# Performance work log

Measured on AMD Instinct MI355X. Metric: run time of the kernel, lower is better.

## Reference

```python
import jax, jax.numpy as jnp
import numpy as np

BN_EPS = 1e-5

def _bn(y, g, b, m, v):
    # inference-mode BatchNorm2d over channel axis 1
    scale = g / jnp.sqrt(v + BN_EPS)
    return (y - m[None, :, None, None]) * scale[None, :, None, None] + b[None, :, None, None]

def setup_inputs() -> dict:
    key = jax.random.key(0)
    ks = jax.random.split(key, 16)
    b, c, h, w = 4, 64, 256, 512
    kc = 32
    return {
        "x": jax.random.normal(ks[0], (b, c, h, w), dtype=jnp.float32),
        "Wq": jax.random.normal(ks[1], (kc, c), dtype=jnp.float32) * 0.05,
        "bnq_g": jax.random.uniform(ks[2], (kc,), dtype=jnp.float32),
        "bnq_b": jax.random.normal(ks[3], (kc,), dtype=jnp.float32) * 0.1,
        "bnq_m": jax.random.normal(ks[4], (kc,), dtype=jnp.float32) * 0.1,
        "bnq_v": jax.random.uniform(ks[5], (kc,), dtype=jnp.float32) + 0.5,
        "Wk": jax.random.normal(ks[6], (kc, c), dtype=jnp.float32) * 0.05,
        "bnk_g": jax.random.uniform(ks[7], (kc,), dtype=jnp.float32),
        "bnk_b": jax.random.normal(ks[8], (kc,), dtype=jnp.float32) * 0.1,
        "bnk_m": jax.random.normal(ks[9], (kc,), dtype=jnp.float32) * 0.1,
        "bnk_v": jax.random.uniform(ks[10], (kc,), dtype=jnp.float32) + 0.5,
        "Wv": jax.random.normal(ks[11], (c, c), dtype=jnp.float32) * 0.05,
        "bv": jax.random.normal(ks[12], (c,), dtype=jnp.float32) * 0.1,
        "gamma": jax.random.normal(ks[13], (1,), dtype=jnp.float32) * 0.1,
    }

def reference(x, Wq, bnq_g, bnq_b, bnq_m, bnq_v, Wk, bnk_g, bnk_b, bnk_m, bnk_v, Wv, bv, gamma):
    # x: [b,c,h,w]. Vertical (height-axis) attention, independent per (batch, column).
    q = _bn(jnp.einsum('kc,bchw->bkhw', Wq, x), bnq_g, bnq_b, bnq_m, bnq_v)  # [b,kc,h,w]
    k = _bn(jnp.einsum('kc,bchw->bkhw', Wk, x), bnk_g, bnk_b, bnk_m, bnk_v)  # [b,kc,h,w]
    # score1 = Q[b,w,h,kc] @ K[b,w,kc,h] -> [b,w,h,h]
    score = jnp.einsum('bkhw,bkgw->bwhg', q, k)
    attn = jax.nn.softmax(score, axis=-1)  # softmax over key height g
    v = jnp.einsum('dc,bchw->bdhw', Wv, x) + bv[None, :, None, None]  # [b,c,h,w]
    buf = jnp.einsum('bwhg,bdgw->bdhw', attn, v)  # [b,c,h,w]
    return gamma * buf + x  # out_add branch
```

## Files before the change

### kernel.cpp

```cpp
#include <hip/hip_runtime.h>
#include <hip/hip_bf16.h>

#define BB 4
#define CC 64
#define HH 256
#define WW 512
#define KCC 32
#define PLANE (HH*WW)

typedef __attribute__((ext_vector_type(8))) __bf16 bf16x8;
typedef __attribute__((ext_vector_type(4))) __bf16 bf16x4;
typedef __attribute__((ext_vector_type(2))) __bf16 bf16x2;
typedef __attribute__((ext_vector_type(4))) float floatx4;

__device__ __forceinline__ float bf2f(unsigned short u) {
    union { unsigned v; float f; } x; x.v = ((unsigned)u) << 16; return x.f;
}

__global__ __launch_bounds__(256, 4)
void proj_kernel(const float* __restrict__ x,
                 const float* __restrict__ Wq, const float* __restrict__ Wk,
                 const float* __restrict__ Wv, const float* __restrict__ bv,
                 const float* __restrict__ bnq_g, const float* __restrict__ bnq_b,
                 const float* __restrict__ bnq_m, const float* __restrict__ bnq_v,
                 const float* __restrict__ bnk_g, const float* __restrict__ bnk_b,
                 const float* __restrict__ bnk_m, const float* __restrict__ bnk_v,
                 unsigned short* __restrict__ Qb, unsigned short* __restrict__ Kb,
                 unsigned short* __restrict__ Vb)
{
    __shared__ __align__(16) unsigned short sX[8 * 256 * 8];
    __shared__ __align__(16) unsigned short sY[4][16 * 40];
    __shared__ float sScale[128], sBias[128];

    const int tid  = threadIdx.x;
    const int lane = tid & 63, wv = tid >> 6;
    const int quad = lane >> 4, lr = lane & 15;
    const int bid  = blockIdx.x;
    const int b = bid >> 9, chunk = bid & 511;
    const int h = chunk >> 1, w0 = (chunk & 1) << 8;

    if (tid < 128) {
        float s, bia;
        if (tid < 32)      { s = bnq_g[tid] * rsqrtf(bnq_v[tid] + 1e-5f); bia = bnq_b[tid] - bnq_m[tid] * s; }
        else if (tid < 64) { int i = tid - 32; s = bnk_g[i] * rsqrtf(bnk_v[i] + 1e-5f); bia = bnk_b[i] - bnk_m[i] * s; }
        else               { s = 1.f; bia = bv[tid - 64]; }
        sScale[tid] = s; sBias[tid] = bia;
    }

    {
        const float* xb = x + (size_t)b * CC * PLANE + h * WW + w0 + tid;
#pragma unroll
        for (int cc = 0; cc < 8; ++cc) {
            bf16x8 v;
#pragma unroll
            for (int j = 0; j < 8; ++j) v[j] = (__bf16)xb[(size_t)(cc * 8 + j) * PLANE];
            *(bf16x8*)&sX[(cc * 256 + tid) * 8] = v;
        }
    }
    __syncthreads();

    const float* Wsrc = (wv == 0) ? Wq : (wv == 1) ? Wk : (Wv + (wv - 2) * 32 * CC);
    bf16x8 wf[2][2];
#pragma unroll
    for (int mt = 0; mt < 2; ++mt)
#pragma unroll
        for (int ks = 0; ks < 2; ++ks) {
            const float* p = Wsrc + (mt * 16 + lr) * CC + ks * 32 + quad * 8;
            bf16x8 v;
#pragma unroll
            for (int j = 0; j < 8; ++j) v[j] = (__bf16)p[j];
            wf[mt][ks] = v;
        }
    float s8[2][4], b8[2][4];
#pragma unroll
    for (int mt = 0; mt < 2; ++mt)
#pragma unroll
        for (int i = 0; i < 4; ++i) {
            int chn = wv * 32 + mt * 16 + quad * 4 + i;
            s8[mt][i] = sScale[chn]; b8[mt][i] = sBias[chn];
        }

    unsigned short* sYw = sY[wv];
    const int p2 = lane >> 2, seg = lane & 3;

    for (int nt = 0; nt < 16; ++nt) {
        bf16x8 xb0 = *(const bf16x8*)&sX[((0 + quad) * 256 + nt * 16 + lr) * 8];
        bf16x8 xb1 = *(const bf16x8*)&sX[((4 + quad) * 256 + nt * 16 + lr) * 8];
#pragma unroll
        for (int mt = 0; mt < 2; ++mt) {
            floatx4 acc = {0.f, 0.f, 0.f, 0.f};
            acc = __builtin_amdgcn_mfma_f32_16x16x32_bf16(wf[mt][0], xb0, acc, 0, 0, 0);
            acc = __builtin_amdgcn_mfma_f32_16x16x32_bf16(wf[mt][1], xb1, acc, 0, 0, 0);
            bf16x4 y;
#pragma unroll
            for (int i = 0; i < 4; ++i) y[i] = (__bf16)(acc[i] * s8[mt][i] + b8[mt][i]);
            *(bf16x4*)&sYw[lr * 40 + mt * 16 + quad * 4] = y;
        }
        uint4 v = *(const uint4*)&sYw[p2 * 40 + seg * 8];
        int w_ = w0 + nt * 16 + p2;
        if (wv == 0)      *(uint4*)&Qb[(size_t)((b * WW + w_) * HH + h) * KCC + seg * 8] = v;
        else if (wv == 1) *(uint4*)&Kb[(size_t)((b * WW + w_) * HH + h) * KCC + seg * 8] = v;
        else              *(uint4*)&Vb[(size_t)((b * WW + w_) * HH + h) * CC + (wv - 2) * 32 + seg * 8] = v;
    }
}

__global__ __launch_bounds__(512, 4)
void attn_kernel(const unsigned short* __restrict__ Qb,
                 const unsigned short* __restrict__ Kb,
                 const unsigned short* __restrict__ Vb,
                 const float* __restrict__ gamma,
                 unsigned short* __restrict__ Ob)
{
    __shared__ __align__(16) unsigned short sVf[16384];
    __shared__ __align__(16) unsigned short sP[8][1280];
    __shared__ float sL[256];

    const int tid = threadIdx.x, lane = tid & 63, wv = tid >> 6;
    const int quad = lane >> 4, lr = lane & 15;
    const int col = blockIdx.x;

    const unsigned short* Qg = Qb + (size_t)col * HH * KCC;
    const unsigned short* Kg = Kb + (size_t)col * HH * KCC;
    const unsigned short* Vg = Vb + (size_t)col * HH * CC;

    bf16x8 qf[2], kf[16];
#pragma unroll
    for (int ht = 0; ht < 2; ++ht)
        qf[ht] = *(const bf16x8*)&Qg[(wv * 32 + ht * 16 + lr) * KCC + quad * 8];
#pragma unroll
    for (int gt = 0; gt < 16; ++gt)
        kf[gt] = *(const bf16x8*)&Kg[(gt * 16 + lr) * KCC + quad * 8];

    unsigned short* sVp = &sP[0][0];
    for (int half = 0; half < 2; ++half) {
#pragma unroll
        for (int it = 0; it < 2; ++it) {
            int idx = it * 512 + tid;
            int gr = idx >> 3, sg = idx & 7;
            *(uint4*)&sVp[gr * CC + sg * 8] =
                *(const uint4*)&Vg[(size_t)(half * 128 + gr) * CC + sg * 8];
        }
        __syncthreads();
#pragma unroll
        for (int it = 0; it < 2; ++it) {
            int id = it * 512 + tid;
            int go = id >> 6, d = id & 63;
            bf16x8 v;
#pragma unroll
            for (int j = 0; j < 8; ++j)
                ((unsigned short*)&v)[j] = sVp[(go * 8 + j) * CC + d];
            *(bf16x8*)&sVf[((half * 16 + go) * 64 + d) * 8] = v;
        }
        __syncthreads();
    }

    floatx4 O[2][4];
#pragma unroll
    for (int a = 0; a < 2; ++a)
#pragma unroll
        for (int dd = 0; dd < 4; ++dd) O[a][dd] = (floatx4){0.f, 0.f, 0.f, 0.f};
    float lpart[2] = {0.f, 0.f};

    unsigned short* sPw = sP[wv];
    const floatx4 zed = {0.f, 0.f, 0.f, 0.f};

#pragma unroll
    for (int ch = 0; ch < 8; ++ch) {
#pragma unroll
        for (int gt = 0; gt < 2; ++gt) {
#pragma unroll
            for (int ht = 0; ht < 2; ++ht) {
                floatx4 s = __builtin_amdgcn_mfma_f32_16x16x32_bf16(kf[ch * 2 + gt], qf[ht], zed, 0, 0, 0);
                float p0 = __expf(s[0]), p1 = __expf(s[1]), p2 = __expf(s[2]), p3 = __expf(s[3]);
                lpart[ht] += (p0 + p1) + (p2 + p3);
                bf16x2 pa = {(__bf16)p0, (__bf16)p1};
                bf16x2 pb = {(__bf16)p2, (__bf16)p3};
                int base = (ht * 16 + lr) * 40 + gt * 16 + quad * 4;
                *(bf16x2*)&sPw[base]     = pa;
                *(bf16x2*)&sPw[base + 2] = pb;
            }
        }
        bf16x8 paf[2];
#pragma unroll
        for (int ht = 0; ht < 2; ++ht)
            paf[ht] = *(const bf16x8*)&sPw[(ht * 16 + lr) * 40 + quad * 8];
#pragma unroll
        for (int dt = 0; dt < 4; ++dt) {
            bf16x8 vf = *(const bf16x8*)&sVf[((ch * 4 + quad) * 64 + dt * 16 + lr) * 8];
#pragma unroll
            for (int ht = 0; ht < 2; ++ht)
                O[ht][dt] = __builtin_amdgcn_mfma_f32_16x16x32_bf16(paf[ht], vf, O[ht][dt], 0, 0, 0);
        }
    }

    const float gm = gamma[0];
#pragma unroll
    for (int ht = 0; ht < 2; ++ht) {
        float l = lpart[ht];
        l += __shfl_xor(l, 16, 64);
        l += __shfl_xor(l, 32, 64);
        if (lane < 16) sL[wv * 32 + ht * 16 + lane] = gm / l;
    }

#pragma unroll
    for (int ht = 0; ht < 2; ++ht) {
        float f0 = sL[wv * 32 + ht * 16 + quad * 4 + 0];
        float f1 = sL[wv * 32 + ht * 16 + quad * 4 + 1];
        float f2 = sL[wv * 32 + ht * 16 + quad * 4 + 2];
        float f3 = sL[wv * 32 + ht * 16 + quad * 4 + 3];
#pragma unroll
        for (int dt = 0; dt < 4; ++dt) {
            floatx4 o = O[ht][dt];
            int cb = dt * 16 + lr;
            *(__bf16*)&sPw[(quad * 4 + 0) * 72 + cb] = (__bf16)(o[0] * f0);
            *(__bf16*)&sPw[(quad * 4 + 1) * 72 + cb] = (__bf16)(o[1] * f1);
            *(__bf16*)&sPw[(quad * 4 + 2) * 72 + cb] = (__bf16)(o[2] * f2);
            *(__bf16*)&sPw[(quad * 4 + 3) * 72 + cb] = (__bf16)(o[3] * f3);
        }
#pragma unroll
        for (int it = 0; it < 2; ++it) {
            int idx = it * 64 + lane;
            int hr = idx >> 3, sg = idx & 7;
            uint4 v = *(const uint4*)&sPw[hr * 72 + sg * 8];
            *(uint4*)&Ob[(size_t)(col * HH + wv * 32 + ht * 16 + hr) * CC + sg * 8] = v;
        }
    }
}

__global__ __launch_bounds__(256)
void add_kernel(const unsigned short* __restrict__ Ob,
                const float* __restrict__ x,
                float* __restrict__ out)
{
    __shared__ __align__(16) unsigned short sT[64 * 72];
    const int tid = threadIdx.x;
    const int bid = blockIdx.x;
    const int b = bid >> 11, rem = bid & 2047, h = rem >> 3, w0 = (rem & 7) << 6;

#pragma unroll
    for (int it = 0; it < 2; ++it) {
        int idx = it * 256 + tid;
        int tw = idx >> 3, sg = idx & 7;
        uint4 v = *(const uint4*)&Ob[(size_t)((b * WW + w0 + tw) * HH + h) * CC + sg * 8];
        *(uint4*)&sT[tw * 72 + sg * 8] = v;
    }
    __syncthreads();

    const int d = tid >> 2, ws = tid & 3;
    const size_t base = ((size_t)(b * CC + d)) * PLANE + h * WW + w0 + ws * 16;
    const float* xp = x + base;
    float* op = out + base;
#pragma unroll
    for (int k = 0; k < 4; ++k) {
        float4 xv = *(const float4*)&xp[k * 4];
        float4 r;
        r.x = bf2f(sT[(ws * 16 + k * 4 + 0) * 72 + d]) + xv.x;
        r.y = bf2f(sT[(ws * 16 + k * 4 + 1) * 72 + d]) + xv.y;
        r.z = bf2f(sT[(ws * 16 + k * 4 + 2) * 72 + d]) + xv.z;
        r.w = bf2f(sT[(ws * 16 + k * 4 + 3) * 72 + d]) + xv.w;
        *(float4*)&op[k * 4] = r;
    }
}

#define KSTR 40
#define VSTR 72
__device__ __forceinline__ float bflo(unsigned u) { union { unsigned v; float f; } x; x.v = u << 16; return x.f; }
__device__ __forceinline__ float bfhi(unsigned u) { union { unsigned v; float f; } x; x.v = u & 0xffff0000u; return x.f; }

__global__ __launch_bounds__(256, 1)
void vattn_fused(const float* __restrict__ x,
                 const float* __restrict__ Wq,
                 const float* __restrict__ bnq_g, const float* __restrict__ bnq_b,
                 const float* __restrict__ bnq_m, const float* __restrict__ bnq_v,
                 const float* __restrict__ Wk,
                 const float* __restrict__ bnk_g, const float* __restrict__ bnk_b,
                 const float* __restrict__ bnk_m, const float* __restrict__ bnk_v,
                 const float* __restrict__ Wv, const float* __restrict__ bv,
                 const float* __restrict__ gamma,
                 float* __restrict__ out)
{
    __shared__ __align__(16) __hip_bfloat16 sK[HH * KSTR];
    __shared__ __align__(16) __hip_bfloat16 sV2[HH * VSTR];
    const int t = threadIdx.x;
    const int bw = blockIdx.x;
    const int b = bw / WW, w = bw % WW;
    const size_t plane = (size_t)HH * WW;
    const float* xp = x + (size_t)b * CC * plane + (size_t)t * WW + w;
    float xr[CC];
#pragma unroll
    for (int c = 0; c < CC; ++c) xr[c] = xp[(size_t)c * plane];
    float qr[KCC];
#pragma unroll
    for (int j = 0; j < KCC; ++j) {
        float aq = 0.f, ak = 0.f;
#pragma unroll
        for (int c = 0; c < CC; ++c) { aq += Wq[j * CC + c] * xr[c]; ak += Wk[j * CC + c] * xr[c]; }
        const float sq = bnq_g[j] * rsqrtf(bnq_v[j] + 1e-5f);
        const float sk = bnk_g[j] * rsqrtf(bnk_v[j] + 1e-5f);
        qr[j] = (aq - bnq_m[j]) * sq + bnq_b[j];
        sK[t * KSTR + j] = __float2bfloat16((ak - bnk_m[j]) * sk + bnk_b[j]);
    }
#pragma unroll
    for (int d = 0; d < CC; ++d) {
        float av = bv[d];
#pragma unroll
        for (int c = 0; c < CC; ++c) av += Wv[d * CC + c] * xr[c];
        sV2[t * VSTR + d] = __float2bfloat16(av);
    }
    __syncthreads();
    float o[CC];
#pragma unroll
    for (int d = 0; d < CC; ++d) o[d] = 0.f;
    float l = 0.f;
    for (int g = 0; g < HH; ++g) {
        const uint4* kp = (const uint4*)(sK + g * KSTR);
        float s = 0.f;
#pragma unroll
        for (int i = 0; i < 4; ++i) {
            const uint4 kk = kp[i];
            s += bflo(kk.x) * qr[i * 8 + 0] + bfhi(kk.x) * qr[i * 8 + 1]
               + bflo(kk.y) * qr[i * 8 + 2] + bfhi(kk.y) * qr[i * 8 + 3]
               + bflo(kk.z) * qr[i * 8 + 4] + bfhi(kk.z) * qr[i * 8 + 5]
               + bflo(kk.w) * qr[i * 8 + 6] + bfhi(kk.w) * qr[i * 8 + 7];
        }
        const float p = __expf(s);
        l += p;
        const uint4* vp = (const uint4*)(sV2 + g * VSTR);
#pragma unroll
        for (int i = 0; i < 8; ++i) {
            const uint4 vv = vp[i];
            o[i * 8 + 0] += p * bflo(vv.x); o[i * 8 + 1] += p * bfhi(vv.x);
            o[i * 8 + 2] += p * bflo(vv.y); o[i * 8 + 3] += p * bfhi(vv.y);
            o[i * 8 + 4] += p * bflo(vv.z); o[i * 8 + 5] += p * bfhi(vv.z);
            o[i * 8 + 6] += p * bflo(vv.w); o[i * 8 + 7] += p * bfhi(vv.w);
        }
    }
    const float gm = gamma[0];
    const float rl = 1.f / l;
    float* op = out + (size_t)b * CC * plane + (size_t)t * WW + w;
#pragma unroll
    for (int d = 0; d < CC; ++d) op[(size_t)d * plane] = gm * (o[d] * rl) + xr[d];
}

extern "C" void kernel_launch(void* const* d_in, const int* in_sizes, int n_in,
                              void* d_out, int out_size, void* d_ws, size_t ws_size,
                              hipStream_t stream) {
    const float* x     = (const float*)d_in[0];
    const float* Wq    = (const float*)d_in[1];
    const float* bnq_g = (const float*)d_in[2];
    const float* bnq_b = (const float*)d_in[3];
    const float* bnq_m = (const float*)d_in[4];
    const float* bnq_v = (const float*)d_in[5];
    const float* Wk    = (const float*)d_in[6];
    const float* bnk_g = (const float*)d_in[7];
    const float* bnk_b = (const float*)d_in[8];
    const float* bnk_m = (const float*)d_in[9];
    const float* bnk_v = (const float*)d_in[10];
    const float* Wv    = (const float*)d_in[11];
    const float* bv    = (const float*)d_in[12];
    const float* gamma = (const float*)d_in[13];
    float* out = (float*)d_out;

    const size_t need = 201326592;
    if (ws_size >= need) {
        unsigned short* Qb = (unsigned short*)d_ws;
        unsigned short* Kb = Qb + 16777216;
        unsigned short* Vb = Kb + 16777216;
        unsigned short* Ob = Vb + 33554432;
        hipLaunchKernelGGL(proj_kernel, dim3(2048), dim3(256), 0, stream,
                           x, Wq, Wk, Wv, bv,
                           bnq_g, bnq_b, bnq_m, bnq_v,
                           bnk_g, bnk_b, bnk_m, bnk_v,
                           Qb, Kb, Vb);
        hipLaunchKernelGGL(attn_kernel, dim3(2048), dim3(512), 0, stream,
                           Qb, Kb, Vb, gamma, Ob);
        hipLaunchKernelGGL(add_kernel, dim3(8192), dim3(256), 0, stream,
                           Ob, x, out);
    } else {
        hipLaunchKernelGGL(vattn_fused, dim3(BB * WW), dim3(HH), 0, stream,
                           x, Wq, bnq_g, bnq_b, bnq_m, bnq_v,
                           Wk, bnk_g, bnk_b, bnk_m, bnk_v,
                           Wv, bv, gamma, out);
    }
}
```

Measured before the change: 423.5 us.

## Tile projection kernel over 16x16 spatial blocks for contiguous Q/K/V stores

```diff
diff --git a/kernel.cpp b/kernel.cpp
--- a/kernel.cpp
+++ b/kernel.cpp
@@ -29,40 +29,37 @@
                  unsigned short* __restrict__ Vb)
 {
     __shared__ __align__(16) unsigned short sX[8 * 256 * 8];
-    __shared__ __align__(16) unsigned short sY[4][16 * 40];
-    __shared__ float sScale[128], sBias[128];
+    __shared__ __align__(16) unsigned short sYQ[16 * 40];
+    __shared__ __align__(16) unsigned short sYK[16 * 40];
+    __shared__ __align__(16) unsigned short sYV[2][16 * 72];
 
     const int tid  = threadIdx.x;
     const int lane = tid & 63, wv = tid >> 6;
     const int quad = lane >> 4, lr = lane & 15;
     const int bid  = blockIdx.x;
-    const int b = bid >> 9, chunk = bid & 511;
-    const int h = chunk >> 1, w0 = (chunk & 1) << 8;
-
-    if (tid < 128) {
-        float s, bia;
-        if (tid < 32)      { s = bnq_g[tid] * rsqrtf(bnq_v[tid] + 1e-5f); bia = bnq_b[tid] - bnq_m[tid] * s; }
-        else if (tid < 64) { int i = tid - 32; s = bnk_g[i] * rsqrtf(bnk_v[i] + 1e-5f); bia = bnk_b[i] - bnk_m[i] * s; }
-        else               { s = 1.f; bia = bv[tid - 64]; }
-        sScale[tid] = s; sBias[tid] = bia;
-    }
+    const int b = bid >> 9, rem = bid & 511;
+    const int h0 = (rem >> 5) << 4;
+    const int w0 = (rem & 31) << 4;
 
     {
-        const float* xb = x + (size_t)b * CC * PLANE + h * WW + w0 + tid;
+        const int lw = tid & 15, lh = tid >> 4;
+        const float* xb = x + (size_t)b * CC * PLANE + (size_t)(h0 + lh) * WW + w0 + lw;
+        const int chs = ((lw << 4) | (lh ^ lw)) * 8;
 #pragma unroll
         for (int cc = 0; cc < 8; ++cc) {
             bf16x8 v;
 #pragma unroll
             for (int j = 0; j < 8; ++j) v[j] = (__bf16)xb[(size_t)(cc * 8 + j) * PLANE];
-            *(bf16x8*)&sX[(cc * 256 + tid) * 8] = v;
-        }
-    }
-    __syncthreads();
-
-    const float* Wsrc = (wv == 0) ? Wq : (wv == 1) ? Wk : (Wv + (wv - 2) * 32 * CC);
-    bf16x8 wf[2][2];
-#pragma unroll
-    for (int mt = 0; mt < 2; ++mt)
+            *(bf16x8*)&sX[cc * 2048 + chs] = v;
+        }
+    }
+
+    const int nmt = (wv >= 2) ? 4 : 2;
+    const float* Wsrc = (wv == 0) ? Wq : (wv == 1) ? Wk : Wv;
+    bf16x8 wf[4][2];
+#pragma unroll
+    for (int mt = 0; mt < 4; ++mt) {
+        if (mt >= nmt) break;
 #pragma unroll
         for (int ks = 0; ks < 2; ++ks) {
             const float* p = Wsrc + (mt * 16 + lr) * CC + ks * 32 + quad * 8;
@@ -71,36 +68,85 @@
             for (int j = 0; j < 8; ++j) v[j] = (__bf16)p[j];
             wf[mt][ks] = v;
         }
-    float s8[2][4], b8[2][4];
-#pragma unroll
-    for (int mt = 0; mt < 2; ++mt)
-#pragma unroll
-        for (int i = 0; i < 4; ++i) {
-            int chn = wv * 32 + mt * 16 + quad * 4 + i;
-            s8[mt][i] = sScale[chn]; b8[mt][i] = sBias[chn];
-        }
-
-    unsigned short* sYw = sY[wv];
-    const int p2 = lane >> 2, seg = lane & 3;
-
-    for (int nt = 0; nt < 16; ++nt) {
-        bf16x8 xb0 = *(const bf16x8*)&sX[((0 + quad) * 256 + nt * 16 + lr) * 8];
-        bf16x8 xb1 = *(const bf16x8*)&sX[((4 + quad) * 256 + nt * 16 + lr) * 8];
-#pragma unroll
-        for (int mt = 0; mt < 2; ++mt) {
-            floatx4 acc = {0.f, 0.f, 0.f, 0.f};
-            acc = __builtin_amdgcn_mfma_f32_16x16x32_bf16(wf[mt][0], xb0, acc, 0, 0, 0);
-            acc = __builtin_amdgcn_mfma_f32_16x16x32_bf16(wf[mt][1], xb1, acc, 0, 0, 0);
-            bf16x4 y;
-#pragma unroll
-            for (int i = 0; i < 4; ++i) y[i] = (__bf16)(acc[i] * s8[mt][i] + b8[mt][i]);
-            *(bf16x4*)&sYw[lr * 40 + mt * 16 + quad * 4] = y;
-        }
-        uint4 v = *(const uint4*)&sYw[p2 * 40 + seg * 8];
-        int w_ = w0 + nt * 16 + p2;
-        if (wv == 0)      *(uint4*)&Qb[(size_t)((b * WW + w_) * HH + h) * KCC + seg * 8] = v;
-        else if (wv == 1) *(uint4*)&Kb[(size_t)((b * WW + w_) * HH + h) * KCC + seg * 8] = v;
-        else              *(uint4*)&Vb[(size_t)((b * WW + w_) * HH + h) * CC + (wv - 2) * 32 + seg * 8] = v;
+    }
+    float s8[2][4], b8[4][4];
+    if (wv == 0) {
+#pragma unroll
+        for (int mt = 0; mt < 2; ++mt)
+#pragma unroll
+            for (int i = 0; i < 4; ++i) {
+                int chn = mt * 16 + quad * 4 + i;
+                float s = bnq_g[chn] * rsqrtf(bnq_v[chn] + 1e-5f);
+                s8[mt][i] = s; b8[mt][i] = bnq_b[chn] - bnq_m[chn] * s;
+            }
+    } else if (wv == 1) {
+#pragma unroll
+        for (int mt = 0; mt < 2; ++mt)
+#pragma unroll
+            for (int i = 0; i < 4; ++i) {
+                int chn = mt * 16 + quad * 4 + i;
+                float s = bnk_g[chn] * rsqrtf(bnk_v[chn] + 1e-5f);
+                s8[mt][i] = s; b8[mt][i] = bnk_b[chn] - bnk_m[chn] * s;
+            }
+    } else {
+#pragma unroll
+        for (int mt = 0; mt < 4; ++mt)
+#pragma unroll
+            for (int i = 0; i < 4; ++i)
+                b8[mt][i] = bv[mt * 16 + quad * 4 + i];
+    }
+    __syncthreads();
+
+    const floatx4 zed = {0.f, 0.f, 0.f, 0.f};
+
+    if (wv < 2) {
+        unsigned short* sYw = (wv == 0) ? sYQ : sYK;
+        unsigned short* Db  = (wv == 0) ? Qb  : Kb;
+        const int p2 = lane >> 2, seg = lane & 3;
+        for (int nt = 0; nt < 16; ++nt) {
+            const int ch = (nt * 16 + (lr ^ nt)) * 8;
+            bf16x8 xb0 = *(const bf16x8*)&sX[quad * 2048 + ch];
+            bf16x8 xb1 = *(const bf16x8*)&sX[(4 + quad) * 2048 + ch];
+#pragma unroll
+            for (int mt = 0; mt < 2; ++mt) {
+                floatx4 acc = zed;
+                acc = __builtin_amdgcn_mfma_f32_16x16x32_bf16(wf[mt][0], xb0, acc, 0, 0, 0);
+                acc = __builtin_amdgcn_mfma_f32_16x16x32_bf16(wf[mt][1], xb1, acc, 0, 0, 0);
+                bf16x4 y;
+#pragma unroll
+                for (int i = 0; i < 4; ++i) y[i] = (__bf16)(acc[i] * s8[mt][i] + b8[mt][i]);
+                *(bf16x4*)&sYw[lr * 40 + mt * 16 + quad * 4] = y;
+            }
+            uint4 v = *(const uint4*)&sYw[p2 * 40 + seg * 8];
+            *(uint4*)&Db[((size_t)(b * WW + w0 + nt) * HH + h0 + p2) * KCC + seg * 8] = v;
+        }
+    } else {
+        unsigned short* sYw = &sYV[wv - 2][0];
+        const int base_nt = (wv - 2) * 8;
+        for (int n8 = 0; n8 < 8; ++n8) {
+            const int nt = base_nt + n8;
+            const int ch = (nt * 16 + (lr ^ nt)) * 8;
+            bf16x8 xb0 = *(const bf16x8*)&sX[quad * 2048 + ch];
+            bf16x8 xb1 = *(const bf16x8*)&sX[(4 + quad) * 2048 + ch];
+#pragma unroll
+            for (int mt = 0; mt < 4; ++mt) {
+                floatx4 acc = zed;
+                acc = __builtin_amdgcn_mfma_f32_16x16x32_bf16(wf[mt][0], xb0, acc, 0, 0, 0);
+                acc = __builtin_amdgcn_mfma_f32_16x16x32_bf16(wf[mt][1], xb1, acc, 0, 0, 0);
+                bf16x4 y;
+#pragma unroll
+                for (int i = 0; i < 4; ++i) y[i] = (__bf16)(acc[i] + b8[mt][i]);
+                *(bf16x4*)&sYw[lr * 72 + mt * 16 + quad * 4] = y;
+            }
+            const size_t vbase = ((size_t)(b * WW + w0 + nt) * HH + h0) * CC;
+#pragma unroll
+            for (int r = 0; r < 2; ++r) {
+                int idx = r * 64 + lane;
+                int pos = idx >> 3, sg = idx & 7;
+                uint4 v = *(const uint4*)&sYw[pos * 72 + sg * 8];
+                *(uint4*)&Vb[vbase + pos * CC + sg * 8] = v;
+            }
+        }
     }
 }
 
```

Result: no change. 421.9 us (-0.4%).
